# Optimization experiments

Measured on AMD Instinct MI355X. Metric: run time of the kernel, lower is better.

Reference implementation:

```python
import jax, jax.numpy as jnp
import numpy as np

N_NODES = 50000
N_EDGES = 800000
IN_FEAT = 128
OUT_FEAT = 128


def setup_inputs() -> dict:
    key = jax.random.key(0)
    k_h, k_src, k_dst, k_w, k_b = jax.random.split(key, 5)
    h = jax.random.normal(k_h, (N_NODES, IN_FEAT), dtype=jnp.float32)
    src = jax.random.randint(k_src, (N_EDGES,), 0, N_NODES, dtype=jnp.int64)
    dst = jax.random.randint(k_dst, (N_EDGES,), 0, N_NODES, dtype=jnp.int64)
    # nn.Linear(2*in_feat, out_feat): weight [out, 2*in], bias [out]
    W = jax.random.normal(k_w, (OUT_FEAT, 2 * IN_FEAT), dtype=jnp.float32) / np.sqrt(2 * IN_FEAT)
    b = jax.random.normal(k_b, (OUT_FEAT,), dtype=jnp.float32) * 0.01
    return {"h": h, "src": src, "dst": dst, "W": W, "b": b}


def reference(h, src, dst, W, b):
    n = h.shape[0]
    # copy_u + mean: gather source features per edge, mean-reduce by destination
    msg = h[src]  # [E, in_feat]
    agg = jax.ops.segment_sum(msg, dst, num_segments=n)  # [N, in_feat]
    deg = jax.ops.segment_sum(jnp.ones((dst.shape[0],), dtype=h.dtype), dst, num_segments=n)
    h_N = agg / jnp.maximum(deg, 1.0)[:, None]  # isolated nodes -> 0 (DGL mean semantics)
    h_total = jnp.concatenate([h, h_N], axis=1)  # [N, 2*in_feat]
    return h_total @ W.T + b
```

## Files before the change

kernel.cpp:

```cpp
#include <hip/hip_runtime.h>
#include <hip/hip_bf16.h>
#include <cstdint>
#include <cstddef>

#define NN     50000
#define NE     800000
#define FIN    128
#define CAP    64
#define NBIN   784
#define CAPBIN 1280
#define SB     157
#define SCT    1024
#define EPT    5
#define PREPB  786

using bf16x8 = __attribute__((ext_vector_type(8))) short;
using f32x4  = __attribute__((ext_vector_type(4))) float;
using f32x2  = __attribute__((ext_vector_type(2))) float;

static const size_t OFF_CUR  = 0;
static const size_t OFF_PART = 800;
static const size_t S_HB  = 2008640;
static const size_t S_HNB = 8408640;
static const size_t S_WB  = 14808640;
static const size_t S_HF8 = 14841408;

__device__ __forceinline__ unsigned f2bf(float f) {
    unsigned u = __float_as_uint(f);
    return (u + 0x7FFFu + ((u >> 16) & 1u)) >> 16;
}

__global__ __launch_bounds__(SCT) void k_ps(
    const float* __restrict__ h, const float* __restrict__ W,
    unsigned* __restrict__ hB, unsigned* __restrict__ WB,
    uint2* __restrict__ hF8,
    const int* __restrict__ src, const int* __restrict__ dst,
    int* __restrict__ bincursor, int* __restrict__ part)
{
    __shared__ int lcur[NBIN];
    __shared__ int lbase[NBIN];
    int blk = blockIdx.x, tid = threadIdx.x;

    if (blk >= SB) {
        int i = (blk - SB) * SCT + tid;
        size_t e = (size_t)i * 8;
        const float* s;
        unsigned* d;
        bool isH = (e < 6400000);
        if (isH) { s = h + e; d = hB + e / 2; }
        else if (e < 6400000 + 32768) { s = W + (e - 6400000); d = WB + (e - 6400000) / 2; }
        else return;
        float4 a = *(const float4*)s;
        float4 b = *(const float4*)(s + 4);
        uint4 o;
        o.x = f2bf(a.x) | (f2bf(a.y) << 16);
        o.y = f2bf(a.z) | (f2bf(a.w) << 16);
        o.z = f2bf(b.x) | (f2bf(b.y) << 16);
        o.w = f2bf(b.z) | (f2bf(b.w) << 16);
        *(uint4*)d = o;
        if (isH) {
            int w0 = __builtin_amdgcn_cvt_pk_fp8_f32(a.x, a.y, 0, false);
            w0     = __builtin_amdgcn_cvt_pk_fp8_f32(a.z, a.w, w0, true);
            int w1 = __builtin_amdgcn_cvt_pk_fp8_f32(b.x, b.y, 0, false);
            w1     = __builtin_amdgcn_cvt_pk_fp8_f32(b.z, b.w, w1, true);
            hF8[e / 8] = make_uint2((unsigned)w0, (unsigned)w1);
        }
        return;
    }

    int b = blk;
    if (tid < NBIN) lcur[tid] = 0;
    __syncthreads();
    int e0 = b * (EPT * SCT);
    int pk[EPT], rk[EPT];
#pragma unroll
    for (int k = 0; k < EPT; ++k) {
        int e = e0 + k * SCT + tid;
        if (e < NE) {
            int d = dst[e];
            int s = src[e];
            int bin = d >> 6;
            pk[k] = s | ((d & 63) << 16) | (bin << 22);
            rk[k] = atomicAdd(&lcur[bin], 1);
        } else {
            pk[k] = -1;
        }
    }
    __syncthreads();
    if (tid < NBIN) {
        int c = lcur[tid];
        lbase[tid] = c ? atomicAdd(&bincursor[tid], c) : 0;
    }
    __syncthreads();
#pragma unroll
    for (int k = 0; k < EPT; ++k) {
        if (pk[k] != -1) {
            int bin = ((unsigned)pk[k]) >> 22;
            int pos = lbase[bin] + rk[k];
            if (pos < CAPBIN)
                part[bin * CAPBIN + pos] = pk[k] & 0x3FFFFF;
        }
    }
}

__device__ __forceinline__ f32x2 fp8lo(unsigned u) {
    return __builtin_amdgcn_cvt_pk_f32_fp8((int)u, false);
}
__device__ __forceinline__ f32x2 fp8hi(unsigned u) {
    return __builtin_amdgcn_cvt_pk_f32_fp8((int)u, true);
}

__global__ __launch_bounds__(256) void k_aggbin(const int* __restrict__ part,
                                                const int* __restrict__ bincursor,
                                                const unsigned* __restrict__ hF8u,
                                                unsigned* __restrict__ hNB2) {
    __shared__ int ldeg[16];
    __shared__ unsigned short bucketL[16 * CAP];
    int blk = blockIdx.x, tid = threadIdx.x;
    int bin = blk >> 2, sub = blk & 3;
    if (tid < 16) ldeg[tid] = 0;
    __syncthreads();
    int cnt = min(bincursor[bin], CAPBIN);
    const int* pj = part + bin * CAPBIN;
    for (int i = tid; i < cnt; i += 256) {
        int v = pj[i];
        int local = (v >> 16) & 63;
        if ((local >> 4) == sub) {
            int l16 = local & 15;
            int slot = atomicAdd(&ldeg[l16], 1);
            if (slot < CAP) bucketL[l16 * CAP + slot] = (unsigned short)v;
        }
    }
    __syncthreads();
    int wave = tid >> 6, lane = tid & 63;
    int halfid = lane >> 5;
    int l32 = lane & 31;
#pragma unroll
    for (int t = 0; t < 4; ++t) {
        int l16 = wave * 4 + t;
        int n = bin * 64 + (sub << 4) + l16;
        if (n >= NN) continue;
        int d = ldeg[l16];
        int c2 = min(d, CAP);
        const unsigned short* bp = &bucketL[l16 * CAP];
        float a0 = 0.f, a1 = 0.f, a2 = 0.f, a3 = 0.f;
        int i = 0;
        for (; i + 16 <= c2; i += 16) {
            unsigned uu[8];
#pragma unroll
            for (int j = 0; j < 8; ++j)
                uu[j] = hF8u[(size_t)bp[i + 2 * j + halfid] * 32 + l32];
#pragma unroll
            for (int j = 0; j < 8; ++j) {
                f32x2 lo = fp8lo(uu[j]);
                f32x2 hi = fp8hi(uu[j]);
                a0 += lo[0]; a1 += lo[1]; a2 += hi[0]; a3 += hi[1];
            }
        }
        for (; i < c2; i += 2) {
            int e = i + halfid;
            unsigned u = 0;
            if (e < c2) u = hF8u[(size_t)bp[e] * 32 + l32];
            f32x2 lo = fp8lo(u);
            f32x2 hi = fp8hi(u);
            a0 += lo[0]; a1 += lo[1]; a2 += hi[0]; a3 += hi[1];
        }
        a0 += __shfl_xor(a0, 32);
        a1 += __shfl_xor(a1, 32);
        a2 += __shfl_xor(a2, 32);
        a3 += __shfl_xor(a3, 32);
        if (halfid == 0) {
            float inv = 1.0f / fmaxf((float)d, 1.0f);
            unsigned p0 = f2bf(a0 * inv) | (f2bf(a1 * inv) << 16);
            unsigned p1 = f2bf(a2 * inv) | (f2bf(a3 * inv) << 16);
            *(uint2*)(hNB2 + (size_t)n * 64 + l32 * 2) = make_uint2(p0, p1);
        }
    }
}

__global__ __launch_bounds__(256) void k_gemm(
    const short* __restrict__ hB, const short* __restrict__ hNB,
    const short* __restrict__ WB, const float* __restrict__ bias,
    float* __restrict__ out)
{
    __shared__ short WL[16384];
    const int tid = threadIdx.x;
    const int jbase = blockIdx.y * 64;

    for (int g = tid; g < 2048; g += 256) {
        int row = g >> 5;
        int c   = g & 31;
        int cs  = (c + row) & 31;
        bf16x8 v = *(const bf16x8*)(WB + (size_t)(jbase + row) * 256 + c * 8);
        *(bf16x8*)(&WL[row * 256 + cs * 8]) = v;
    }
    __syncthreads();

    const int wave = tid >> 6;
    const int lane = tid & 63;
    const int q    = lane >> 4;
    const int ln   = lane & 15;
    const int mbase = (blockIdx.x * 4 + wave) * 16;
    int node = mbase + ln;
    if (node >= NN) node = NN - 1;

    f32x4 acc[4];
#pragma unroll
    for (int t = 0; t < 4; ++t) acc[t] = (f32x4){0.f, 0.f, 0.f, 0.f};

#pragma unroll
    for (int k0 = 0; k0 < 8; ++k0) {
        int ck = k0 * 4 + q;
        const short* ap = (k0 < 4) ? (hB  + (size_t)node * 128 + ck * 8)
                                   : (hNB + (size_t)node * 128 + (ck - 16) * 8);
        bf16x8 afr = *(const bf16x8*)ap;
#pragma unroll
        for (int t = 0; t < 4; ++t) {
            int row = t * 16 + ln;
            int cs  = (ck + row) & 31;
            bf16x8 bfr = *(const bf16x8*)(&WL[row * 256 + cs * 8]);
            acc[t] = __builtin_amdgcn_mfma_f32_16x16x32_bf16(afr, bfr, acc[t], 0, 0, 0);
        }
    }

#pragma unroll
    for (int t = 0; t < 4; ++t) {
        float bv = bias[jbase + t * 16 + ln];
#pragma unroll
        for (int r = 0; r < 4; ++r) {
            int m = mbase + q * 4 + r;
            if (m < NN)
                out[(size_t)m * FIN + jbase + t * 16 + ln] = acc[t][r] + bv;
        }
    }
}

extern "C" void kernel_launch(void* const* d_in, const int* in_sizes, int n_in,
                              void* d_out, int out_size, void* d_ws, size_t ws_size,
                              hipStream_t stream) {
    const float* h   = (const float*)d_in[0];
    const int*   src = (const int*)d_in[1];
    const int*   dst = (const int*)d_in[2];
    const float* W   = (const float*)d_in[3];
    const float* b   = (const float*)d_in[4];
    float* out = (float*)d_out;

    int*   wsI = (int*)d_ws;
    short* wsS = (short*)d_ws;

    int* bincursor = wsI + OFF_CUR;
    int* part      = wsI + OFF_PART;
    short* hB      = wsS + S_HB;
    short* hNB     = wsS + S_HNB;
    short* WB      = wsS + S_WB;
    const unsigned* hF8u = (const unsigned*)(wsS + S_HF8);

    hipMemsetAsync(bincursor, 0, NBIN * sizeof(int), stream);
    k_ps     <<<SB + PREPB, SCT, 0, stream>>>(
        h, W, (unsigned*)hB, (unsigned*)WB, (uint2*)(wsS + S_HF8),
        src, dst, bincursor, part);
    k_aggbin <<<NBIN * 4, 256, 0, stream>>>(part, bincursor, hF8u, (unsigned*)hNB);
    k_gemm   <<<dim3((NN + 63) / 64, 2), 256, 0, stream>>>(hB, hNB, WB, b, out);
}
```

Before: 140.1 us.

## Fuse neighbor aggregation with GEMM, keeping mean features in shared memory

Merges the binned mean-aggregation kernel and the bf16 MFMA GEMM into one kernel. Each block aggregates 32 destination nodes into a swizzled shared-memory tile and multiplies it, together with the self features, against the full W held in LDS. This removes the hNB global round trip and one kernel launch. In exchange every block loads all of W (64KB LDS) plus buckets, which lowers occupancy, and the part array is scanned with 2 blocks per bin instead of 4.

```diff
diff --git a/kernel.cpp b/kernel.cpp
--- a/kernel.cpp
+++ b/kernel.cpp
@@ -13,6 +13,7 @@
 #define SCT    1024
 #define EPT    5
 #define PREPB  786
+#define NBLK2  1563
 
 using bf16x8 = __attribute__((ext_vector_type(8))) short;
 using f32x4  = __attribute__((ext_vector_type(4))) float;
@@ -110,39 +111,56 @@
     return __builtin_amdgcn_cvt_pk_f32_fp8((int)u, true);
 }
 
-__global__ __launch_bounds__(256) void k_aggbin(const int* __restrict__ part,
-                                                const int* __restrict__ bincursor,
-                                                const unsigned* __restrict__ hF8u,
-                                                unsigned* __restrict__ hNB2) {
-    __shared__ int ldeg[16];
-    __shared__ unsigned short bucketL[16 * CAP];
-    int blk = blockIdx.x, tid = threadIdx.x;
-    int bin = blk >> 2, sub = blk & 3;
-    if (tid < 16) ldeg[tid] = 0;
-    __syncthreads();
+__global__ __launch_bounds__(256) void k_fused(
+    const int* __restrict__ part,
+    const int* __restrict__ bincursor,
+    const unsigned* __restrict__ hF8u,
+    const short* __restrict__ hB,
+    const short* __restrict__ WB,
+    const float* __restrict__ bias,
+    float* __restrict__ out)
+{
+    __shared__ short WL[32768];
+    __shared__ unsigned short bucketL[32 * CAP];
+    __shared__ short hNL[32 * 128];
+    __shared__ int ldeg[32];
+
+    const int blk = blockIdx.x, tid = threadIdx.x;
+    const int bin = blk >> 1, sub = blk & 1;
+
+    for (int g = tid; g < 4096; g += 256) {
+        int row = g >> 5;
+        int c   = g & 31;
+        int cs  = (c + row) & 31;
+        bf16x8 v = *(const bf16x8*)(WB + (size_t)row * 256 + c * 8);
+        *(bf16x8*)(&WL[row * 256 + cs * 8]) = v;
+    }
+
+    if (tid < 32) ldeg[tid] = 0;
+    __syncthreads();
+
     int cnt = min(bincursor[bin], CAPBIN);
     const int* pj = part + bin * CAPBIN;
     for (int i = tid; i < cnt; i += 256) {
         int v = pj[i];
         int local = (v >> 16) & 63;
-        if ((local >> 4) == sub) {
-            int l16 = local & 15;
-            int slot = atomicAdd(&ldeg[l16], 1);
-            if (slot < CAP) bucketL[l16 * CAP + slot] = (unsigned short)v;
-        }
-    }
-    __syncthreads();
-    int wave = tid >> 6, lane = tid & 63;
-    int halfid = lane >> 5;
-    int l32 = lane & 31;
-#pragma unroll
-    for (int t = 0; t < 4; ++t) {
-        int l16 = wave * 4 + t;
-        int n = bin * 64 + (sub << 4) + l16;
-        if (n >= NN) continue;
-        int d = ldeg[l16];
+        if ((local >> 5) == sub) {
+            int l5 = local & 31;
+            int slot = atomicAdd(&ldeg[l5], 1);
+            if (slot < CAP) bucketL[l5 * CAP + slot] = (unsigned short)v;
+        }
+    }
+    __syncthreads();
+
+    const int wave = tid >> 6, lane = tid & 63;
+    const int halfid = lane >> 5;
+    const int l32 = lane & 31;
+#pragma unroll
+    for (int t = 0; t < 8; ++t) {
+        int l5 = wave * 8 + t;
+        int d = ldeg[l5];
         int c2 = min(d, CAP);
-        const unsigned short* bp = &bucketL[l16 * CAP];
+        const unsigned short* bp = &bucketL[l5 * CAP];
         float a0 = 0.f, a1 = 0.f, a2 = 0.f, a3 = 0.f;
         int i = 0;
         for (; i + 16 <= c2; i += 16) {
@@ -173,36 +191,20 @@
             float inv = 1.0f / fmaxf((float)d, 1.0f);
             unsigned p0 = f2bf(a0 * inv) | (f2bf(a1 * inv) << 16);
             unsigned p1 = f2bf(a2 * inv) | (f2bf(a3 * inv) << 16);
-            *(uint2*)(hNB2 + (size_t)n * 64 + l32 * 2) = make_uint2(p0, p1);
-        }
-    }
-}
-
-__global__ __launch_bounds__(256) void k_gemm(
-    const short* __restrict__ hB, const short* __restrict__ hNB,
-    const short* __restrict__ WB, const float* __restrict__ bias,
-    float* __restrict__ out)
-{
-    __shared__ short WL[16384];
-    const int tid = threadIdx.x;
-    const int jbase = blockIdx.y * 64;
-
-    for (int g = tid; g < 2048; g += 256) {
-        int row = g >> 5;
-        int c   = g & 31;
-        int cs  = (c + row) & 31;
-        bf16x8 v = *(const bf16x8*)(WB + (size_t)(jbase + row) * 256 + c * 8);
-        *(bf16x8*)(&WL[row * 256 + cs * 8]) = v;
-    }
-    __syncthreads();
-
-    const int wave = tid >> 6;
-    const int lane = tid & 63;
-    const int q    = lane >> 4;
-    const int ln   = lane & 15;
-    const int mbase = (blockIdx.x * 4 + wave) * 16;
-    int node = mbase + ln;
+            int c  = l32 >> 1;
+            int cs = (c + l5) & 15;
+            *(uint2*)(&hNL[l5 * 128 + cs * 8 + (l32 & 1) * 4]) = make_uint2(p0, p1);
+        }
+    }
+    __syncthreads();
+
+    const int q  = lane >> 4;
+    const int ln = lane & 15;
+    const int msub  = wave >> 1;
+    const int nhalf = wave & 1;
+    int node = blk * 32 + msub * 16 + ln;
     if (node >= NN) node = NN - 1;
+    const int mrow = msub * 16 + ln;
 
     f32x4 acc[4];
 #pragma unroll
@@ -211,26 +213,32 @@
 #pragma unroll
     for (int k0 = 0; k0 < 8; ++k0) {
         int ck = k0 * 4 + q;
-        const short* ap = (k0 < 4) ? (hB  + (size_t)node * 128 + ck * 8)
-                                   : (hNB + (size_t)node * 128 + (ck - 16) * 8);
-        bf16x8 afr = *(const bf16x8*)ap;
+        bf16x8 afr;
+        if (k0 < 4) {
+            afr = *(const bf16x8*)(hB + (size_t)node * 128 + ck * 8);
+        } else {
+            int ckn = ck - 16;
+            int csn = (ckn + mrow) & 15;
+            afr = *(const bf16x8*)(&hNL[mrow * 128 + csn * 8]);
+        }
 #pragma unroll
         for (int t = 0; t < 4; ++t) {
-            int row = t * 16 + ln;
-            int cs  = (ck + row) & 31;
-            bf16x8 bfr = *(const bf16x8*)(&WL[row * 256 + cs * 8]);
+            int rowj = nhalf * 64 + t * 16 + ln;
+            int cs   = (ck + rowj) & 31;
+            bf16x8 bfr = *(const bf16x8*)(&WL[rowj * 256 + cs * 8]);
             acc[t] = __builtin_amdgcn_mfma_f32_16x16x32_bf16(afr, bfr, acc[t], 0, 0, 0);
         }
     }
 
 #pragma unroll
     for (int t = 0; t < 4; ++t) {
-        float bv = bias[jbase + t * 16 + ln];
+        int j = nhalf * 64 + t * 16 + ln;
+        float bv = bias[j];
 #pragma unroll
         for (int r = 0; r < 4; ++r) {
-            int m = mbase + q * 4 + r;
+            int m = blk * 32 + msub * 16 + q * 4 + r;
             if (m < NN)
-                out[(size_t)m * FIN + jbase + t * 16 + ln] = acc[t][r] + bv;
+                out[(size_t)m * FIN + j] = acc[t][r] + bv;
         }
     }
 }
@@ -251,14 +259,12 @@
     int* bincursor = wsI + OFF_CUR;
     int* part      = wsI + OFF_PART;
     short* hB      = wsS + S_HB;
-    short* hNB     = wsS + S_HNB;
     short* WB      = wsS + S_WB;
     const unsigned* hF8u = (const unsigned*)(wsS + S_HF8);
 
     hipMemsetAsync(bincursor, 0, NBIN * sizeof(int), stream);
-    k_ps     <<<SB + PREPB, SCT, 0, stream>>>(
+    k_ps    <<<SB + PREPB, SCT, 0, stream>>>(
         h, W, (unsigned*)hB, (unsigned*)WB, (uint2*)(wsS + S_HF8),
         src, dst, bincursor, part);
-    k_aggbin <<<NBIN * 4, 256, 0, stream>>>(part, bincursor, hF8u, (unsigned*)hNB);
-    k_gemm   <<<dim3((NN + 63) / 64, 2), 256, 0, stream>>>(hB, hNB, WB, b, out);
-}
+    k_fused <<<NBLK2, 256, 0, stream>>>(part, bincursor, hF8u, hB, WB, b, out);
+}
```

After: 191.7 us. +36.9%, slower.
